# Kernel tuning notes

Hardware: AMD Instinct MI355X
Metric: run time of the kernel (lower is better)

## Reference

```python
import jax, jax.numpy as jnp
import numpy as np

N_NODES = 50000
N_EDGES = 800000
HIDDEN = 128


def setup_inputs() -> dict:
    key = jax.random.key(0)
    ks = jax.random.split(key, 8)
    node_feat = jax.random.normal(ks[0], (N_NODES, HIDDEN), dtype=jnp.float32)
    edge_feat = jax.random.normal(ks[1], (N_EDGES, HIDDEN), dtype=jnp.float32)
    edge_src = jax.random.randint(ks[2], (N_EDGES,), 0, N_NODES, dtype=jnp.int32)
    edge_dst = jax.random.randint(ks[3], (N_EDGES,), 0, N_NODES, dtype=jnp.int32)
    # MLP params: Linear(h, 2h) -> ReLU -> Linear(2h, h); Kaiming-ish scale
    w1 = jax.random.normal(ks[4], (HIDDEN, 2 * HIDDEN), dtype=jnp.float32) * (1.0 / np.sqrt(HIDDEN))
    b1 = jnp.zeros((2 * HIDDEN,), dtype=jnp.float32)
    w2 = jax.random.normal(ks[5], (2 * HIDDEN, HIDDEN), dtype=jnp.float32) * (1.0 / np.sqrt(2 * HIDDEN))
    b2 = jnp.zeros((HIDDEN,), dtype=jnp.float32)
    return {"node_feat": node_feat, "edge_feat": edge_feat,
            "edge_src": edge_src, "edge_dst": edge_dst,
            "w1": w1, "b1": b1, "w2": w2, "b2": b2}


def reference(node_feat, edge_feat, edge_src, edge_dst, w1, b1, w2, b2):
    # Message: gather src node features per edge, add edge features
    msg = node_feat[edge_src] + edge_feat                     # [E, H]
    # Reduce: scatter-sum messages into destination nodes
    agg = jax.ops.segment_sum(msg, edge_dst, num_segments=node_feat.shape[0])  # [N, H]
    # 2-layer MLP with ReLU
    h = jax.nn.relu(agg @ w1 + b1)                            # [N, 2H]
    out = h @ w2 + b2                                         # [N, H]
    return out
```

## Files before the change

### kernel.cpp

```cpp
#include <hip/hip_runtime.h>


constexpr int NN = 50000;
constexpr int NE = 800000;
constexpr int H  = 128;
constexpr int H2 = 256;

typedef short short8_t __attribute__((ext_vector_type(8)));
typedef float f32x4    __attribute__((ext_vector_type(4)));

__device__ inline short f2bf(float f) {
    union { float f; unsigned u; } c; c.f = f;
    unsigned r = c.u + 0x7FFF + ((c.u >> 16) & 1);
    return (short)(r >> 16);
}

__global__ __launch_bounds__(256) void zero_kernel(int4* __restrict__ p, int n4)
{
    int i = blockIdx.x * blockDim.x + threadIdx.x;
    if (i < n4) p[i] = make_int4(0, 0, 0, 0);
}

__global__ __launch_bounds__(256) void count_kernel(
    const int* __restrict__ edge_dst, int* __restrict__ count)
{
    int e = blockIdx.x * blockDim.x + threadIdx.x;
    if (e < NE) atomicAdd(&count[edge_dst[e]], 1);
}

__global__ __launch_bounds__(256) void scan1_kernel(
    const int* __restrict__ count, int* __restrict__ bsum)
{
    __shared__ int red[256];
    const int t = threadIdx.x;
    const int i = blockIdx.x * 256 + t;
    red[t] = (i < NN) ? count[i] : 0;
    __syncthreads();
    for (int s = 128; s > 0; s >>= 1) {
        if (t < s) red[t] += red[t + s];
        __syncthreads();
    }
    if (t == 0) bsum[blockIdx.x] = red[0];
}

__global__ __launch_bounds__(256) void scan2_kernel(
    const int* __restrict__ bsum, int* __restrict__ bexc, int nb)
{
    __shared__ int s[256];
    const int t = threadIdx.x;
    s[t] = (t < nb) ? bsum[t] : 0;
    __syncthreads();
    for (int off = 1; off < 256; off <<= 1) {
        int v = (t >= off) ? s[t - off] : 0;
        __syncthreads();
        s[t] += v;
        __syncthreads();
    }
    if (t < nb) bexc[t] = (t == 0) ? 0 : s[t - 1];
}

__global__ __launch_bounds__(256) void scan3_kernel(
    const int* __restrict__ count, const int* __restrict__ bexc,
    int* __restrict__ offsets)
{
    __shared__ int s[256];
    const int t = threadIdx.x;
    const int i = blockIdx.x * 256 + t;
    const int c = (i < NN) ? count[i] : 0;
    s[t] = c;
    __syncthreads();
    for (int off = 1; off < 256; off <<= 1) {
        int v = (t >= off) ? s[t - off] : 0;
        __syncthreads();
        s[t] += v;
        __syncthreads();
    }
    if (i < NN) {
        const int excl = bexc[blockIdx.x] + s[t] - c;
        offsets[i] = excl;
        if (i == NN - 1) offsets[NN] = excl + c;
    }
}

__global__ __launch_bounds__(256) void place_kernel(
    const int* __restrict__ edge_dst, const int* __restrict__ edge_src,
    const int* __restrict__ offsets,
    int* __restrict__ cursor, int2* __restrict__ sorted_es)
{
    int e = blockIdx.x * blockDim.x + threadIdx.x;
    if (e < NE) {
        int d = edge_dst[e];
        int pos = offsets[d] + atomicAdd(&cursor[d], 1);
        sorted_es[pos] = make_int2(e, edge_src[e]);
    }
}

__global__ __launch_bounds__(256) void pack_kernel(
    const float* __restrict__ w1, const float* __restrict__ w2,
    short* __restrict__ w1p, short* __restrict__ w2p)
{
    int i = blockIdx.x * 256 + threadIdx.x;
    if (i < 32768) {
        {
            int j = i & 7, l = (i >> 3) & 63, ct = (i >> 9) & 15, kk = i >> 13;
            w1p[i] = f2bf(w1[(kk * 32 + (l >> 4) * 8 + j) * H2 + ct * 16 + (l & 15)]);
        }
        {
            int j = i & 7, l = (i >> 3) & 63, ct = (i >> 9) & 7, kk = i >> 12;
            w2p[i] = f2bf(w2[(kk * 32 + (l >> 4) * 8 + j) * H + ct * 16 + (l & 15)]);
        }
    }
}

__global__ __launch_bounds__(256) void gather_kernel(
    const float* __restrict__ node_feat,
    const float* __restrict__ edge_feat,
    const int2*  __restrict__ sorted_es,
    const int*   __restrict__ offsets,
    short*       __restrict__ aggb)
{
    const int node = blockIdx.x * 4 + (threadIdx.x >> 6);
    const int co   = (threadIdx.x & 63) * 2;
    const int start = offsets[node];
    const int end   = offsets[node + 1];
    float ax = 0.f, ay = 0.f;
    int i = start;
    if ((i & 1) && i < end) {
        const int2 es = sorted_es[i];
        const float2 ef = *(const float2*)(edge_feat + (size_t)es.x * H + co);
        const float2 nf = *(const float2*)(node_feat + (size_t)es.y * H + co);
        ax += ef.x + nf.x;  ay += ef.y + nf.y;
        ++i;
    }
    for (; i + 4 <= end; i += 4) {
        const int4 p0 = *(const int4*)&sorted_es[i];
        const int4 p1 = *(const int4*)&sorted_es[i + 2];
        const float2 e0 = *(const float2*)(edge_feat + (size_t)p0.x * H + co);
        const float2 n0 = *(const float2*)(node_feat + (size_t)p0.y * H + co);
        const float2 e1 = *(const float2*)(edge_feat + (size_t)p0.z * H + co);
        const float2 n1 = *(const float2*)(node_feat + (size_t)p0.w * H + co);
        const float2 e2 = *(const float2*)(edge_feat + (size_t)p1.x * H + co);
        const float2 n2 = *(const float2*)(node_feat + (size_t)p1.y * H + co);
        const float2 e3 = *(const float2*)(edge_feat + (size_t)p1.z * H + co);
        const float2 n3 = *(const float2*)(node_feat + (size_t)p1.w * H + co);
        ax += e0.x + n0.x;  ay += e0.y + n0.y;
        ax += e1.x + n1.x;  ay += e1.y + n1.y;
        ax += e2.x + n2.x;  ay += e2.y + n2.y;
        ax += e3.x + n3.x;  ay += e3.y + n3.y;
    }
    for (; i + 2 <= end; i += 2) {
        const int4 p = *(const int4*)&sorted_es[i];
        const float2 e0 = *(const float2*)(edge_feat + (size_t)p.x * H + co);
        const float2 n0 = *(const float2*)(node_feat + (size_t)p.y * H + co);
        const float2 e1 = *(const float2*)(edge_feat + (size_t)p.z * H + co);
        const float2 n1 = *(const float2*)(node_feat + (size_t)p.w * H + co);
        ax += e0.x + n0.x;  ay += e0.y + n0.y;
        ax += e1.x + n1.x;  ay += e1.y + n1.y;
    }
    if (i < end) {
        const int2 es = sorted_es[i];
        const float2 ef = *(const float2*)(edge_feat + (size_t)es.x * H + co);
        const float2 nf = *(const float2*)(node_feat + (size_t)es.y * H + co);
        ax += ef.x + nf.x;  ay += ef.y + nf.y;
    }
    const unsigned pk = (unsigned)(unsigned short)f2bf(ax)
                      | ((unsigned)(unsigned short)f2bf(ay) << 16);
    *(unsigned*)(aggb + (size_t)node * H + co) = pk;
}

__global__ __launch_bounds__(256) void l1_kernel(
    const short* __restrict__ aggb, const short* __restrict__ w1p,
    const float* __restrict__ b1, short* __restrict__ hb)
{
    __shared__ short s_c[4][16][H2];
    const int t = threadIdx.x;
    const int wid = t >> 6, l = t & 63;
    const int lrow = l & 15, lk = l >> 4;
    const long long mrow = (long long)blockIdx.x * 64 + wid * 16;

    f32x4 acc[16];
    #pragma unroll
    for (int ct = 0; ct < 16; ++ct) acc[ct] = (f32x4){0.f, 0.f, 0.f, 0.f};

    const short8_t* bfr = (const short8_t*)w1p;
    #pragma unroll
    for (int kk = 0; kk < 4; ++kk) {
        short8_t a = {0, 0, 0, 0, 0, 0, 0, 0};
        const long long ar = mrow + lrow;
        if (ar < NN)
            a = *(const short8_t*)(aggb + ar * H + kk * 32 + lk * 8);
        #pragma unroll
        for (int ct = 0; ct < 16; ++ct) {
            const short8_t b = bfr[(kk * 16 + ct) * 64 + l];
            acc[ct] = __builtin_amdgcn_mfma_f32_16x16x32_bf16(a, b, acc[ct], 0, 0, 0);
        }
    }

    #pragma unroll
    for (int ct = 0; ct < 16; ++ct) {
        const float b = b1[ct * 16 + lrow];
        #pragma unroll
        for (int r = 0; r < 4; ++r)
            s_c[wid][lk * 4 + r][ct * 16 + lrow] = f2bf(acc[ct][r] + b > 0.f ? acc[ct][r] + b : 0.f);
    }
    __syncthreads();

    const short* reg = &s_c[wid][0][0];
    #pragma unroll
    for (int it = 0; it < 8; ++it) {
        const int off = it * 64 + l;
        const long long row = mrow + (off >> 5);
        if (row < NN) {
            const short8_t v = ((const short8_t*)reg)[off];
            *(short8_t*)(hb + row * H2 + (off & 31) * 8) = v;
        }
    }
}

__global__ __launch_bounds__(256) void l2_kernel(
    const short* __restrict__ hb, const short* __restrict__ w2p,
    const float* __restrict__ b2, float* __restrict__ out)
{
    __shared__ float s_c[4][16][H];
    const int t = threadIdx.x;
    const int wid = t >> 6, l = t & 63;
    const int lrow = l & 15, lk = l >> 4;
    const long long mrow = (long long)blockIdx.x * 64 + wid * 16;

    f32x4 acc[8];
    #pragma unroll
    for (int ct = 0; ct < 8; ++ct) acc[ct] = (f32x4){0.f, 0.f, 0.f, 0.f};

    const short8_t* bfr = (const short8_t*)w2p;
    #pragma unroll
    for (int kk = 0; kk < 8; ++kk) {
        short8_t a = {0, 0, 0, 0, 0, 0, 0, 0};
        const long long ar = mrow + lrow;
        if (ar < NN)
            a = *(const short8_t*)(hb + ar * H2 + kk * 32 + lk * 8);
        #pragma unroll
        for (int ct = 0; ct < 8; ++ct) {
            const short8_t b = bfr[(kk * 8 + ct) * 64 + l];
            acc[ct] = __builtin_amdgcn_mfma_f32_16x16x32_bf16(a, b, acc[ct], 0, 0, 0);
        }
    }

    #pragma unroll
    for (int ct = 0; ct < 8; ++ct) {
        const float b = b2[ct * 16 + lrow];
        #pragma unroll
        for (int r = 0; r < 4; ++r)
            s_c[wid][lk * 4 + r][ct * 16 + lrow] = acc[ct][r] + b;
    }
    __syncthreads();

    const float* reg = &s_c[wid][0][0];
    #pragma unroll
    for (int it = 0; it < 8; ++it) {
        const int off = it * 64 + l;
        const long long row = mrow + (off >> 5);
        if (row < NN) {
            const float4 v = ((const float4*)reg)[off];
            *(float4*)(out + row * H + (off & 31) * 4) = v;
        }
    }
}

__global__ __launch_bounds__(256) void scatter_kernel(
    const float* __restrict__ node_feat,
    const float* __restrict__ edge_feat,
    const int*   __restrict__ edge_src,
    const int*   __restrict__ edge_dst,
    float*       __restrict__ agg)
{
    long long tid = (long long)blockIdx.x * blockDim.x + threadIdx.x;
    const long long total = (long long)NE * 32;
    if (tid >= total) return;
    int e = (int)(tid >> 5);
    int q = (int)((tid & 31) << 2);
    int s = edge_src[e];
    int d = edge_dst[e];
    const float4 nf = *(const float4*)(node_feat + (long long)s * H + q);
    const float4 ef = *(const float4*)(edge_feat + (long long)e * H + q);
    float* dst = agg + (long long)d * H + q;
    atomicAdd(dst + 0, nf.x + ef.x);
    atomicAdd(dst + 1, nf.y + ef.y);
    atomicAdd(dst + 2, nf.z + ef.z);
    atomicAdd(dst + 3, nf.w + ef.w);
}

__global__ __launch_bounds__(256) void mlp_simple_kernel(
    const float* __restrict__ agg,
    const float* __restrict__ w1, const float* __restrict__ b1,
    const float* __restrict__ w2, const float* __restrict__ b2,
    float*       __restrict__ out)
{
    constexpr int NPB = 16;
    __shared__ float s_in[NPB][H];
    __shared__ float s_h [NPB][H2];
    const int t = threadIdx.x;
    const long long base = (long long)blockIdx.x * NPB;
    {
        const float4* src = (const float4*)(agg + base * H);
        float4* dst = (float4*)(&s_in[0][0]);
        dst[t]       = src[t];
        dst[t + 256] = src[t + 256];
    }
    __syncthreads();
    float acc[NPB];
    {
        const float b = b1[t];
        #pragma unroll
        for (int n = 0; n < NPB; ++n) acc[n] = b;
    }
    #pragma unroll 4
    for (int k = 0; k < H; ++k) {
        const float w = w1[k * H2 + t];
        #pragma unroll
        for (int n = 0; n < NPB; ++n) acc[n] = fmaf(s_in[n][k], w, acc[n]);
    }
    #pragma unroll
    for (int n = 0; n < NPB; ++n) s_h[n][t] = fmaxf(acc[n], 0.0f);
    __syncthreads();
    const int j = t & (H - 1);
    const int g = t >> 7;
    float acc2[NPB / 2];
    {
        const float b = b2[j];
        #pragma unroll
        for (int n = 0; n < NPB / 2; ++n) acc2[n] = b;
    }
    #pragma unroll 4
    for (int k = 0; k < H2; ++k) {
        const float w = w2[k * H + j];
        #pragma unroll
        for (int n = 0; n < NPB / 2; ++n)
            acc2[n] = fmaf(s_h[g * (NPB / 2) + n][k], w, acc2[n]);
    }
    #pragma unroll
    for (int n = 0; n < NPB / 2; ++n)
        out[(base + g * (NPB / 2) + n) * H + j] = acc2[n];
}

__global__ __launch_bounds__(256) void zero_agg_kernel(float4* __restrict__ p, int n4)
{
    int i = blockIdx.x * blockDim.x + threadIdx.x;
    if (i < n4) p[i] = make_float4(0.f, 0.f, 0.f, 0.f);
}

extern "C" void kernel_launch(void* const* d_in, const int* in_sizes, int n_in,
                              void* d_out, int out_size, void* d_ws, size_t ws_size,
                              hipStream_t stream)
{
    const float* node_feat = (const float*)d_in[0];
    const float* edge_feat = (const float*)d_in[1];
    const int*   edge_src  = (const int*)  d_in[2];
    const int*   edge_dst  = (const int*)  d_in[3];
    const float* w1 = (const float*)d_in[4];
    const float* b1 = (const float*)d_in[5];
    const float* w2 = (const float*)d_in[6];
    const float* b2 = (const float*)d_in[7];
    float* out = (float*)d_out;

    const int NB = (NN + 255) / 256;

    const size_t count_b  = ((size_t)NN * 4 + 255) & ~(size_t)255;
    const size_t cursor_b = count_b;
    const size_t offs_b   = (((size_t)NN + 1) * 4 + 255) & ~(size_t)255;
    const size_t bsum_b   = ((size_t)NB * 4 + 255) & ~(size_t)255;
    const size_t bexc_b   = bsum_b;
    const size_t es_b     = ((size_t)NE * 8 + 255) & ~(size_t)255;
    const size_t w1p_b    = (size_t)32768 * 2;
    const size_t w2p_b    = (size_t)32768 * 2;
    const size_t aggb_b   = ((size_t)NN * H * 2 + 255) & ~(size_t)255;
    const size_t hb_b     = ((size_t)NN * H2 * 2 + 255) & ~(size_t)255;
    const size_t need     = count_b + cursor_b + offs_b + bsum_b + bexc_b
                          + es_b + w1p_b + w2p_b + aggb_b + hb_b;

    if (ws_size >= need) {
        char* p = (char*)d_ws;
        int*   count     = (int*)p;              p += count_b;
        int*   cursor    = (int*)p;              p += cursor_b;
        int*   offsets   = (int*)p;              p += offs_b;
        int*   bsum      = (int*)p;              p += bsum_b;
        int*   bexc      = (int*)p;              p += bexc_b;
        int2*  sorted_es = (int2*)p;             p += es_b;
        short* w1p       = (short*)p;            p += w1p_b;
        short* w2p       = (short*)p;            p += w2p_b;
        short* aggb      = (short*)p;            p += aggb_b;
        short* hb        = (short*)p;

        {
            const int n4 = (int)((count_b + cursor_b) / 16);
            zero_kernel<<<(n4 + 255) / 256, 256, 0, stream>>>((int4*)d_ws, n4);
        }

        const int eb = 256, eg = (NE + eb - 1) / eb;
        count_kernel<<<eg, eb, 0, stream>>>(edge_dst, count);
        scan1_kernel<<<NB, 256, 0, stream>>>(count, bsum);
        scan2_kernel<<<1, 256, 0, stream>>>(bsum, bexc, NB);
        scan3_kernel<<<NB, 256, 0, stream>>>(count, bexc, offsets);
        place_kernel<<<eg, eb, 0, stream>>>(edge_dst, edge_src, offsets, cursor, sorted_es);
        pack_kernel<<<128, 256, 0, stream>>>(w1, w2, w1p, w2p);
        gather_kernel<<<NN / 4, 256, 0, stream>>>(
            node_feat, edge_feat, sorted_es, offsets, aggb);
        const int gemm_grid = (NN + 63) / 64;
        l1_kernel<<<gemm_grid, 256, 0, stream>>>(aggb, w1p, b1, hb);
        l2_kernel<<<gemm_grid, 256, 0, stream>>>(hb, w2p, b2, out);
    } else {
        const size_t agg_bytes = (size_t)NN * H * sizeof(float);
        float* agg = (ws_size >= agg_bytes) ? (float*)d_ws : out;
        {
            const int n4 = (int)(agg_bytes / 16);
            zero_agg_kernel<<<(n4 + 255) / 256, 256, 0, stream>>>((float4*)agg, n4);
        }
        const long long total = (long long)NE * 32;
        const int block = 256;
        const int grid  = (int)((total + block - 1) / block);
        scatter_kernel<<<grid, block, 0, stream>>>(
            node_feat, edge_feat, edge_src, edge_dst, agg);
        mlp_simple_kernel<<<NN / 16, 256, 0, stream>>>(agg, w1, b1, w2, b2, out);
    }
}
```

Before: 260.0 us.

## Fuse MLP layers into one kernel and add nontemporal loads with index prefetch

Merges the two GEMM kernels into a single kernel that keeps the bf16 hidden activations in padded shared memory, so the 50000x256 intermediate is never written to or read back from global memory. The gather kernel now uses nontemporal loads for edge features and sorted index pairs, and software-prefetches the next group of index pairs. The count and place kernels also read the edge index arrays with nontemporal loads. The fused kernel needs more shared memory per block, which may limit occupancy. The GEMMs are a small part of the total next to the memory-bound gather.

After: 267.6 us. 1.03x slower.

```diff
diff --git a/kernel.cpp b/kernel.cpp
--- a/kernel.cpp
+++ b/kernel.cpp
@@ -5,9 +5,13 @@
 constexpr int NE = 800000;
 constexpr int H  = 128;
 constexpr int H2 = 256;
+constexpr int SHP = 264;
 
 typedef short short8_t __attribute__((ext_vector_type(8)));
 typedef float f32x4    __attribute__((ext_vector_type(4)));
+typedef float f32x2    __attribute__((ext_vector_type(2)));
+typedef int   i32x4    __attribute__((ext_vector_type(4)));
+typedef int   i32x2    __attribute__((ext_vector_type(2)));
 
 __device__ inline short f2bf(float f) {
     union { float f; unsigned u; } c; c.f = f;
@@ -15,6 +19,10 @@
     return (short)(r >> 16);
 }
 
+__device__ inline f32x2 nt2(const float* p) {
+    return __builtin_nontemporal_load((const f32x2*)p);
+}
+
 __global__ __launch_bounds__(256) void zero_kernel(int4* __restrict__ p, int n4)
 {
     int i = blockIdx.x * blockDim.x + threadIdx.x;
@@ -25,7 +33,10 @@
     const int* __restrict__ edge_dst, int* __restrict__ count)
 {
     int e = blockIdx.x * blockDim.x + threadIdx.x;
-    if (e < NE) atomicAdd(&count[edge_dst[e]], 1);
+    if (e < NE) {
+        const int d = __builtin_nontemporal_load(&edge_dst[e]);
+        atomicAdd(&count[d], 1);
+    }
 }
 
 __global__ __launch_bounds__(256) void scan1_kernel(
@@ -89,9 +100,10 @@
 {
     int e = blockIdx.x * blockDim.x + threadIdx.x;
     if (e < NE) {
-        int d = edge_dst[e];
+        const int d = __builtin_nontemporal_load(&edge_dst[e]);
+        const int s = __builtin_nontemporal_load(&edge_src[e]);
         int pos = offsets[d] + atomicAdd(&cursor[d], 1);
-        sorted_es[pos] = make_int2(e, edge_src[e]);
+        sorted_es[pos] = make_int2(e, s);
     }
 }
 
@@ -127,39 +139,40 @@
     int i = start;
     if ((i & 1) && i < end) {
         const int2 es = sorted_es[i];
-        const float2 ef = *(const float2*)(edge_feat + (size_t)es.x * H + co);
+        const f32x2  ef = nt2(edge_feat + (size_t)es.x * H + co);
         const float2 nf = *(const float2*)(node_feat + (size_t)es.y * H + co);
         ax += ef.x + nf.x;  ay += ef.y + nf.y;
         ++i;
     }
-    for (; i + 4 <= end; i += 4) {
-        const int4 p0 = *(const int4*)&sorted_es[i];
-        const int4 p1 = *(const int4*)&sorted_es[i + 2];
-        const float2 e0 = *(const float2*)(edge_feat + (size_t)p0.x * H + co);
-        const float2 n0 = *(const float2*)(node_feat + (size_t)p0.y * H + co);
-        const float2 e1 = *(const float2*)(edge_feat + (size_t)p0.z * H + co);
-        const float2 n1 = *(const float2*)(node_feat + (size_t)p0.w * H + co);
-        const float2 e2 = *(const float2*)(edge_feat + (size_t)p1.x * H + co);
-        const float2 n2 = *(const float2*)(node_feat + (size_t)p1.y * H + co);
-        const float2 e3 = *(const float2*)(edge_feat + (size_t)p1.z * H + co);
-        const float2 n3 = *(const float2*)(node_feat + (size_t)p1.w * H + co);
+    const int ng = (end - i) >> 2;
+    i32x4 c0 = {0,0,0,0}, c1 = {0,0,0,0};
+    if (ng > 0) {
+        c0 = __builtin_nontemporal_load((const i32x4*)&sorted_es[i]);
+        c1 = __builtin_nontemporal_load((const i32x4*)&sorted_es[i + 2]);
+    }
+    for (int g = 0; g < ng; ++g) {
+        const i32x4 q0 = c0, q1 = c1;
+        if (g + 1 < ng) {
+            c0 = __builtin_nontemporal_load((const i32x4*)&sorted_es[i + 4]);
+            c1 = __builtin_nontemporal_load((const i32x4*)&sorted_es[i + 6]);
+        }
+        const f32x2  e0 = nt2(edge_feat + (size_t)q0.x * H + co);
+        const float2 n0 = *(const float2*)(node_feat + (size_t)q0.y * H + co);
+        const f32x2  e1 = nt2(edge_feat + (size_t)q0.z * H + co);
+        const float2 n1 = *(const float2*)(node_feat + (size_t)q0.w * H + co);
+        const f32x2  e2 = nt2(edge_feat + (size_t)q1.x * H + co);
+        const float2 n2 = *(const float2*)(node_feat + (size_t)q1.y * H + co);
+        const f32x2  e3 = nt2(edge_feat + (size_t)q1.z * H + co);
+        const float2 n3 = *(const float2*)(node_feat + (size_t)q1.w * H + co);
         ax += e0.x + n0.x;  ay += e0.y + n0.y;
         ax += e1.x + n1.x;  ay += e1.y + n1.y;
         ax += e2.x + n2.x;  ay += e2.y + n2.y;
         ax += e3.x + n3.x;  ay += e3.y + n3.y;
-    }
-    for (; i + 2 <= end; i += 2) {
-        const int4 p = *(const int4*)&sorted_es[i];
-        const float2 e0 = *(const float2*)(edge_feat + (size_t)p.x * H + co);
-        const float2 n0 = *(const float2*)(node_feat + (size_t)p.y * H + co);
-        const float2 e1 = *(const float2*)(edge_feat + (size_t)p.z * H + co);
-        const float2 n1 = *(const float2*)(node_feat + (size_t)p.w * H + co);
-        ax += e0.x + n0.x;  ay += e0.y + n0.y;
-        ax += e1.x + n1.x;  ay += e1.y + n1.y;
-    }
-    if (i < end) {
+        i += 4;
+    }
+    for (; i < end; ++i) {
         const int2 es = sorted_es[i];
-        const float2 ef = *(const float2*)(edge_feat + (size_t)es.x * H + co);
+        const f32x2  ef = nt2(edge_feat + (size_t)es.x * H + co);
         const float2 nf = *(const float2*)(node_feat + (size_t)es.y * H + co);
         ax += ef.x + nf.x;  ay += ef.y + nf.y;
     }
@@ -168,99 +181,73 @@
     *(unsigned*)(aggb + (size_t)node * H + co) = pk;
 }
 
-__global__ __launch_bounds__(256) void l1_kernel(
+__global__ __launch_bounds__(256) void mlp_kernel(
     const short* __restrict__ aggb, const short* __restrict__ w1p,
-    const float* __restrict__ b1, short* __restrict__ hb)
-{
-    __shared__ short s_c[4][16][H2];
+    const short* __restrict__ w2p,  const float* __restrict__ b1,
+    const float* __restrict__ b2,   float* __restrict__ out)
+{
+    __shared__ short smem[4 * 16 * SHP];
     const int t = threadIdx.x;
     const int wid = t >> 6, l = t & 63;
     const int lrow = l & 15, lk = l >> 4;
     const long long mrow = (long long)blockIdx.x * 64 + wid * 16;
+    short* s_h = &smem[wid * 16 * SHP];
 
     f32x4 acc[16];
     #pragma unroll
     for (int ct = 0; ct < 16; ++ct) acc[ct] = (f32x4){0.f, 0.f, 0.f, 0.f};
-
-    const short8_t* bfr = (const short8_t*)w1p;
+    const short8_t* bfr1 = (const short8_t*)w1p;
     #pragma unroll
     for (int kk = 0; kk < 4; ++kk) {
         short8_t a = {0, 0, 0, 0, 0, 0, 0, 0};
-        const long long ar = mrow + lrow;
-        if (ar < NN)
-            a = *(const short8_t*)(aggb + ar * H + kk * 32 + lk * 8);
-        #pragma unroll
-        for (int ct = 0; ct < 16; ++ct) {
-            const short8_t b = bfr[(kk * 16 + ct) * 64 + l];
-            acc[ct] = __builtin_amdgcn_mfma_f32_16x16x32_bf16(a, b, acc[ct], 0, 0, 0);
-        }
-    }
-
+        if (mrow + lrow < NN)
+            a = *(const short8_t*)(aggb + (mrow + lrow) * H + kk * 32 + lk * 8);
+        #pragma unroll
+        for (int ct = 0; ct < 16; ++ct)
+            acc[ct] = __builtin_amdgcn_mfma_f32_16x16x32_bf16(
+                a, bfr1[(kk * 16 + ct) * 64 + l], acc[ct], 0, 0, 0);
+    }
     #pragma unroll
     for (int ct = 0; ct < 16; ++ct) {
         const float b = b1[ct * 16 + lrow];
         #pragma unroll
+        for (int r = 0; r < 4; ++r) {
+            float v = acc[ct][r] + b;
+            s_h[(lk * 4 + r) * SHP + ct * 16 + lrow] = f2bf(v > 0.f ? v : 0.f);
+        }
+    }
+    __syncthreads();
+
+    f32x4 acc2[8];
+    #pragma unroll
+    for (int ct = 0; ct < 8; ++ct) acc2[ct] = (f32x4){0.f, 0.f, 0.f, 0.f};
+    const short8_t* bfr2 = (const short8_t*)w2p;
+    #pragma unroll
+    for (int kk = 0; kk < 8; ++kk) {
+        const short8_t a = *(const short8_t*)&s_h[lrow * SHP + kk * 32 + lk * 8];
+        #pragma unroll
+        for (int ct = 0; ct < 8; ++ct)
+            acc2[ct] = __builtin_amdgcn_mfma_f32_16x16x32_bf16(
+                a, bfr2[(kk * 8 + ct) * 64 + l], acc2[ct], 0, 0, 0);
+    }
+    __syncthreads();
+
+    float* sc = (float*)s_h;
+    #pragma unroll
+    for (int ct = 0; ct < 8; ++ct) {
+        const float b = b2[ct * 16 + lrow];
+        #pragma unroll
         for (int r = 0; r < 4; ++r)
-            s_c[wid][lk * 4 + r][ct * 16 + lrow] = f2bf(acc[ct][r] + b > 0.f ? acc[ct][r] + b : 0.f);
-    }
-    __syncthreads();
-
-    const short* reg = &s_c[wid][0][0];
+            sc[(lk * 4 + r) * 132 + ct * 16 + lrow] = acc2[ct][r] + b;
+    }
+    __syncthreads();
+
     #pragma unroll
     for (int it = 0; it < 8; ++it) {
         const int off = it * 64 + l;
         const long long row = mrow + (off >> 5);
         if (row < NN) {
-            const short8_t v = ((const short8_t*)reg)[off];
-            *(short8_t*)(hb + row * H2 + (off & 31) * 8) = v;
-        }
-    }
-}
-
-__global__ __launch_bounds__(256) void l2_kernel(
-    const short* __restrict__ hb, const short* __restrict__ w2p,
-    const float* __restrict__ b2, float* __restrict__ out)
-{
-    __shared__ float s_c[4][16][H];
-    const int t = threadIdx.x;
-    const int wid = t >> 6, l = t & 63;
-    const int lrow = l & 15, lk = l >> 4;
-    const long long mrow = (long long)blockIdx.x * 64 + wid * 16;
-
-    f32x4 acc[8];
-    #pragma unroll
-    for (int ct = 0; ct < 8; ++ct) acc[ct] = (f32x4){0.f, 0.f, 0.f, 0.f};
-
-    const short8_t* bfr = (const short8_t*)w2p;
-    #pragma unroll
-    for (int kk = 0; kk < 8; ++kk) {
-        short8_t a = {0, 0, 0, 0, 0, 0, 0, 0};
-        const long long ar = mrow + lrow;
-        if (ar < NN)
-            a = *(const short8_t*)(hb + ar * H2 + kk * 32 + lk * 8);
-        #pragma unroll
-        for (int ct = 0; ct < 8; ++ct) {
-            const short8_t b = bfr[(kk * 8 + ct) * 64 + l];
-            acc[ct] = __builtin_amdgcn_mfma_f32_16x16x32_bf16(a, b, acc[ct], 0, 0, 0);
-        }
-    }
-
-    #pragma unroll
-    for (int ct = 0; ct < 8; ++ct) {
-        const float b = b2[ct * 16 + lrow];
-        #pragma unroll
-        for (int r = 0; r < 4; ++r)
-            s_c[wid][lk * 4 + r][ct * 16 + lrow] = acc[ct][r] + b;
-    }
-    __syncthreads();
-
-    const float* reg = &s_c[wid][0][0];
-    #pragma unroll
-    for (int it = 0; it < 8; ++it) {
-        const int off = it * 64 + l;
-        const long long row = mrow + (off >> 5);
-        if (row < NN) {
-            const float4 v = ((const float4*)reg)[off];
+            const float4 v = *(const float4*)&sc[(off >> 5) * 132 + (off & 31) * 4];
             *(float4*)(out + row * H + (off & 31) * 4) = v;
         }
     }
@@ -373,9 +360,8 @@
     const size_t w1p_b    = (size_t)32768 * 2;
     const size_t w2p_b    = (size_t)32768 * 2;
     const size_t aggb_b   = ((size_t)NN * H * 2 + 255) & ~(size_t)255;
-    const size_t hb_b     = ((size_t)NN * H2 * 2 + 255) & ~(size_t)255;
     const size_t need     = count_b + cursor_b + offs_b + bsum_b + bexc_b
-                          + es_b + w1p_b + w2p_b + aggb_b + hb_b;
+                          + es_b + w1p_b + w2p_b + aggb_b;
 
     if (ws_size >= need) {
         char* p = (char*)d_ws;
@@ -387,8 +373,7 @@
         int2*  sorted_es = (int2*)p;             p += es_b;
         short* w1p       = (short*)p;            p += w1p_b;
         short* w2p       = (short*)p;            p += w2p_b;
-        short* aggb      = (short*)p;            p += aggb_b;
-        short* hb        = (short*)p;
+        short* aggb      = (short*)p;
 
         {
             const int n4 = (int)((count_b + cursor_b) / 16);
@@ -404,9 +389,8 @@
         pack_kernel<<<128, 256, 0, stream>>>(w1, w2, w1p, w2p);
         gather_kernel<<<NN / 4, 256, 0, stream>>>(
             node_feat, edge_feat, sorted_es, offsets, aggb);
-        const int gemm_grid = (NN + 63) / 64;
-        l1_kernel<<<gemm_grid, 256, 0, stream>>>(aggb, w1p, b1, hb);
-        l2_kernel<<<gemm_grid, 256, 0, stream>>>(hb, w2p, b2, out);
+        const int mlp_grid = (NN + 63) / 64;
+        mlp_kernel<<<mlp_grid, 256, 0, stream>>>(aggb, w1p, w2p, b1, b2, out);
     } else {
         const size_t agg_bytes = (size_t)NN * H * sizeof(float);
         float* agg = (ws_size >= agg_bytes) ? (float*)d_ws : out;
```
